# Performance work log

Hardware: AMD Instinct MI355X
Metric: run time of the kernel (lower is better)

Reference implementation:

```python
import jax, jax.numpy as jnp
import numpy as np

EPS = 1e-5
K_NN = 16

def _lin1d(x, W, b):
    # 1x1 Conv1d: x (B,C,N) -> (B,O,N)
    return jnp.einsum('oc,bcn->bon', W, x) + b[None, :, None]

def _lin2d(x, W, b):
    # 1x1 Conv2d: x (B,C,N,K) -> (B,O,N,K)
    return jnp.einsum('oc,bcnk->bonk', W, x) + b[None, :, None, None]

def _bn2d(x, gamma, beta):
    # train-mode BatchNorm2d over (B, N, K) per channel
    mean = jnp.mean(x, axis=(0, 2, 3), keepdims=True)
    var = jnp.var(x, axis=(0, 2, 3), keepdims=True)
    xh = (x - mean) * jax.lax.rsqrt(var + EPS)
    return gamma[None, :, None, None] * xh + beta[None, :, None, None]

def _knn_idx(pq, ps, k):
    # pq (B,3,N), ps (B,3,M) -> idx (B,N,K) of k nearest support points
    d2 = (jnp.sum(pq * pq, axis=1)[:, :, None]
          + jnp.sum(ps * ps, axis=1)[:, None, :]
          - 2.0 * jnp.einsum('bcn,bcm->bnm', pq, ps))
    _, idx = jax.lax.top_k(-d2, k)
    return idx

def _group(x, idx):
    # x (B,C,M), idx (B,N,K) -> (B,C,N,K)
    return jnp.take_along_axis(x[:, :, None, :], idx[:, None, :, :], axis=3)

def setup_inputs() -> dict:
    key = jax.random.key(0)
    ks = jax.random.split(key, 20)
    B, C, D, N, M, H = 4, 128, 64, 2048, 2048, 256
    s = lambda k, shape, scale: (jax.random.normal(k, shape, dtype=jnp.float32) * scale)
    return {
        'pq': s(ks[0], (B, 3, N), 1.0),
        'fq': s(ks[1], (B, C, N), 1.0),
        'ps': s(ks[2], (B, 3, M), 1.0),
        'fs': s(ks[3], (B, C, M), 1.0),
        'Wq': s(ks[4], (D, C), 0.05), 'bq': jnp.zeros((D,), jnp.float32),
        'Wk': s(ks[5], (D, C), 0.05), 'bk': jnp.zeros((D,), jnp.float32),
        'Wv': s(ks[6], (D, C), 0.05), 'bv': jnp.zeros((D,), jnp.float32),
        'Wp1': s(ks[7], (D, 3), 0.2), 'bp1': jnp.zeros((D,), jnp.float32),
        'gp': jnp.ones((D,), jnp.float32), 'btp': jnp.zeros((D,), jnp.float32),
        'Wp2': s(ks[8], (D, D), 0.05), 'bp2': jnp.zeros((D,), jnp.float32),
        'Wa1': s(ks[9], (H, D), 0.05), 'ba1': jnp.zeros((H,), jnp.float32),
        'ga': jnp.ones((H,), jnp.float32), 'bta': jnp.zeros((H,), jnp.float32),
        'Wa2': s(ks[10], (D, H), 0.05), 'ba2': jnp.zeros((D,), jnp.float32),
        'We': s(ks[11], (C, D), 0.05), 'be': jnp.zeros((C,), jnp.float32),
    }

def reference(pq, fq, ps, fs, Wq, bq, Wk, bk, Wv, bv,
              Wp1, bp1, gp, btp, Wp2, bp2,
              Wa1, ba1, ga, bta, Wa2, ba2, We, be):
    identity = fq
    q = _lin1d(fq, Wq, bq)          # (B,D,N)
    k = _lin1d(fs, Wk, bk)          # (B,D,M)
    v = _lin1d(fs, Wv, bv)          # (B,D,M)
    idx = _knn_idx(pq, ps, K_NN)    # (B,N,K)
    key_g = _group(k, idx)          # (B,D,N,K)
    qk_rel = q[:, :, :, None] - key_g
    pos_rel = pq[:, :, :, None] - _group(ps, idx)  # (B,3,N,K)
    # pos_mlp: conv-bn-relu-conv
    pe = _lin2d(pos_rel, Wp1, bp1)
    pe = jax.nn.relu(_bn2d(pe, gp, btp))
    pe = _lin2d(pe, Wp2, bp2)       # (B,D,N,K)
    # attn_mlp: conv-bn-relu-conv
    a = _lin2d(qk_rel + pe, Wa1, ba1)
    a = jax.nn.relu(_bn2d(a, ga, bta))
    a = _lin2d(a, Wa2, ba2)         # (B,D,N,K)
    attn = jax.nn.softmax(a, axis=-1)
    val = _group(v, idx) + pe       # (B,D,N,K)
    agg = jnp.einsum('bcnk,bcnk->bcn', attn, val)
    return _lin1d(agg, We, be) + identity
```

## Files before the change

kernel.cpp:

```cpp
#include <hip/hip_runtime.h>
#include <stdint.h>

#define NN 2048
#define MM 2048
#define NSAMP 131072

typedef float  fv4 __attribute__((ext_vector_type(4)));
typedef short  bfv8 __attribute__((ext_vector_type(8)));
typedef short  bfv4 __attribute__((ext_vector_type(4)));
typedef unsigned short u16;
typedef unsigned long long u64;

__device__ inline u16 f2bf(float x){
  unsigned u = __float_as_uint(x);
  return (u16)((u + 0x7FFFu + ((u>>16)&1u)) >> 16);
}
__device__ inline float bf2f(u16 u){ return __uint_as_float(((unsigned)u)<<16); }
#define MFMA16 __builtin_amdgcn_mfma_f32_16x16x32_bf16

__global__ __launch_bounds__(256) void k_prep(
    const float* __restrict__ Wq, const float* __restrict__ Wk, const float* __restrict__ Wv,
    const float* __restrict__ Wp2, const float* __restrict__ Wa2, const float* __restrict__ We,
    const float* __restrict__ ps,
    u16* __restrict__ Wqbf, u16* __restrict__ Wkbf, u16* __restrict__ Wvbf,
    u16* __restrict__ Wp2bf, u16* __restrict__ Wa2bf, u16* __restrict__ Webf,
    fv4* __restrict__ psP) {
  int gid = blockIdx.x * 256 + threadIdx.x;
  if (gid < 8192)  { Wqbf[gid] = f2bf(Wq[gid]); Wkbf[gid] = f2bf(Wk[gid]);
                     Wvbf[gid] = f2bf(Wv[gid]); Webf[gid] = f2bf(We[gid]); }
  if (gid < 4096)  Wp2bf[gid] = f2bf(Wp2[gid]);
  if (gid < 16384) Wa2bf[gid] = f2bf(Wa2[gid]);
  if (gid < 8192)  { int b = gid >> 11, m = gid & 2047;
    float x = ps[(b*3+0)*MM + m], y = ps[(b*3+1)*MM + m], z = ps[(b*3+2)*MM + m];
    fv4 p; p.x = x; p.y = y; p.z = z; p.w = x*x + y*y + z*z;
    psP[gid] = p; }
}

__global__ __launch_bounds__(256) void k_qkv(
    const float* __restrict__ fq, const float* __restrict__ fs,
    const u16* __restrict__ Wqbf, const u16* __restrict__ Wkbf, const u16* __restrict__ Wvbf,
    const float* __restrict__ bq, const float* __restrict__ bk, const float* __restrict__ bv,
    float* __restrict__ qT, float* __restrict__ kT, float* __restrict__ vT) {
  __shared__ u16 tile[2][32 * 136];
  int bid = blockIdx.x;
  int b = bid >> 6, p0 = (bid & 63) * 32;
  int t = threadIdx.x;
  int w = t >> 6, l = t & 63, lq = l >> 4, ln = l & 15;
  {
    int cq = t >> 3, n4 = (t & 7) * 4;
    #pragma unroll
    for (int it = 0; it < 4; ++it) {
      int c = it * 32 + cq;
      fv4 vq = *(const fv4*)&fq[(b*128 + c)*2048 + p0 + n4];
      fv4 vs = *(const fv4*)&fs[(b*128 + c)*2048 + p0 + n4];
      #pragma unroll
      for (int j = 0; j < 4; ++j) {
        tile[0][(n4 + j)*136 + c] = f2bf(vq[j]);
        tile[1][(n4 + j)*136 + c] = f2bf(vs[j]);
      }
    }
  }
  bfv8 A[3][4];
  #pragma unroll
  for (int mat = 0; mat < 3; ++mat) {
    const u16* W = mat == 0 ? Wqbf : (mat == 1 ? Wkbf : Wvbf);
    #pragma unroll
    for (int kk = 0; kk < 4; ++kk)
      A[mat][kk] = *(const bfv8*)(W + (w*16 + ln)*128 + kk*32 + lq*8);
  }
  __syncthreads();
  fv4 acc[3][2];
  #pragma unroll
  for (int mat = 0; mat < 3; ++mat) {
    const u16* tl = tile[mat == 0 ? 0 : 1];
    #pragma unroll
    for (int nt = 0; nt < 2; ++nt) {
      fv4 a = {0.f,0.f,0.f,0.f};
      #pragma unroll
      for (int kk = 0; kk < 4; ++kk) {
        bfv8 bb = *(const bfv8*)&tl[(nt*16 + ln)*136 + kk*32 + lq*8];
        a = MFMA16(A[mat][kk], bb, a, 0, 0, 0);
      }
      acc[mat][nt] = a;
    }
  }
  #pragma unroll
  for (int mat = 0; mat < 3; ++mat) {
    float* dst = mat == 0 ? qT : (mat == 1 ? kT : vT);
    const float* bia = mat == 0 ? bq : (mat == 1 ? bk : bv);
    fv4 bq4 = *(const fv4*)&bia[w*16 + lq*4];
    #pragma unroll
    for (int nt = 0; nt < 2; ++nt) {
      fv4 o = acc[mat][nt] + bq4;
      *(fv4*)&dst[(b*NN + p0 + nt*16 + ln)*64 + w*16 + lq*4] = o;
    }
  }
}

__global__ __launch_bounds__(128) void k_knn(
    const float* __restrict__ pq, const fv4* __restrict__ psP,
    int* __restrict__ idxb, float* __restrict__ posPart) {
  __shared__ u64 winLDS[2][64];
  __shared__ float sacc[2][9];
  int t = threadIdx.x, w = t >> 6, lane = t & 63;
  int qi = blockIdx.x * 2 + w;
  int b = qi >> 11, n = qi & 2047;
  const float* pqb = pq + b * 3 * NN;
  const fv4* psb = psP + b * 2048;
  float qx = pqb[n], qy = pqb[NN + n], qz = pqb[2 * NN + n];
  float qq = qx * qx + qy * qy + qz * qz;

  u64 A[16], Bv[16];
  #pragma unroll
  for (int j = 0; j < 16; ++j) {
    int m = lane + 64 * j;
    fv4 P = psb[m];
    float d2 = qq + P.w - 2.f * (qx * P.x + qy * P.y + qz * P.z);
    unsigned bu = __float_as_uint(d2);
    bu = (bu & 0x80000000u) ? ~bu : (bu | 0x80000000u);
    A[j] = (((u64)bu) << 32) | (unsigned)m;
  }
  #pragma unroll
  for (int j = 0; j < 16; ++j) {
    int m = lane + 64 * (j + 16);
    fv4 P = psb[m];
    float d2 = qq + P.w - 2.f * (qx * P.x + qy * P.y + qz * P.z);
    unsigned bu = __float_as_uint(d2);
    bu = (bu & 0x80000000u) ? ~bu : (bu | 0x80000000u);
    Bv[j] = (((u64)bu) << 32) | (unsigned)m;
  }
  #pragma unroll
  for (int k = 2; k <= 16; k <<= 1) {
    #pragma unroll
    for (int j = k >> 1; j > 0; j >>= 1) {
      #pragma unroll
      for (int i = 0; i < 16; ++i) {
        int l2 = i ^ j;
        if (l2 > i) {
          bool up = ((i & k) == 0);
          { u64 x = A[i], y = A[l2];
            bool sw = up ? (y < x) : (x < y);
            A[i] = sw ? y : x;  A[l2] = sw ? x : y; }
          { u64 x = Bv[i], y = Bv[l2];
            bool sw = up ? (y < x) : (x < y);
            Bv[i] = sw ? y : x; Bv[l2] = sw ? x : y; }
        }
      }
    }
  }
  #pragma unroll
  for (int i = 0; i < 16; ++i) {
    u64 y = Bv[15 - i];
    A[i] = A[i] < y ? A[i] : y;
  }
  #pragma unroll
  for (int j = 8; j > 0; j >>= 1) {
    #pragma unroll
    for (int i = 0; i < 16; ++i) {
      int l2 = i ^ j;
      if (l2 > i) {
        u64 x = A[i], y = A[l2];
        bool sw = (y < x);
        A[i] = sw ? y : x;  A[l2] = sw ? x : y;
      }
    }
  }
  for (int r = 0; r < 16; ++r) {
    u64 v = A[0];
    u64 mv = v;
    #pragma unroll
    for (int off = 1; off <= 8; off <<= 1) {
      u64 o = __shfl_xor(mv, off, 64);
      mv = o < mv ? o : mv;
    }
    bool pop = (v == mv);
    #pragma unroll
    for (int i = 0; i < 15; ++i) A[i] = pop ? A[i+1] : A[i];
    A[15] = pop ? ~0ULL : A[15];
    if ((lane & 15) == 0) winLDS[w][(lane >> 4) * 16 + r] = mv;
  }
  u64 e = winLDS[w][lane];
  #pragma unroll
  for (int k = 2; k <= 64; k <<= 1) {
    #pragma unroll
    for (int j = k >> 1; j > 0; j >>= 1) {
      u64 x = __shfl_xor(e, j, 64);
      u64 lo = e < x ? e : x, hi = e < x ? x : e;
      bool up = ((lane & k) == 0);
      bool takeLo = (((lane & j) == 0) == up);
      e = takeLo ? lo : hi;
    }
  }
  if (lane < 16) idxb[qi * 16 + lane] = (int)(e & 0xFFFFFFFFu);
  winLDS[w][lane] = e;
  float s0=0.f,s1=0.f,s2=0.f,s3=0.f,s4=0.f,s5=0.f,s6=0.f,s7=0.f,s8=0.f;
  #pragma unroll 4
  for (int r = 0; r < 16; ++r) {
    unsigned m = (unsigned)(winLDS[w][r] & 0xFFFFFFFFu);
    fv4 P = psb[m];
    float r0 = qx - P.x, r1 = qy - P.y, r2 = qz - P.z;
    s0 += r0; s1 += r1; s2 += r2;
    s3 += r0*r0; s4 += r0*r1; s5 += r0*r2;
    s6 += r1*r1; s7 += r1*r2; s8 += r2*r2;
  }
  if (lane == 0) {
    sacc[w][0]=s0; sacc[w][1]=s1; sacc[w][2]=s2; sacc[w][3]=s3; sacc[w][4]=s4;
    sacc[w][5]=s5; sacc[w][6]=s6; sacc[w][7]=s7; sacc[w][8]=s8;
  }
  __syncthreads();
  if (t < 9) posPart[blockIdx.x * 12 + t] = sacc[0][t] + sacc[1][t];
}

__global__ __launch_bounds__(256) void k_posfinal(
    const float* __restrict__ Wp1, const float* __restrict__ bp1,
    const float* __restrict__ gp, const float* __restrict__ btp,
    const float* __restrict__ posPart, float* __restrict__ Wp1f, float* __restrict__ bp1f) {
  __shared__ float red[4][9];
  __shared__ float st[9];
  int t = threadIdx.x;
  int w = t >> 6, lane = t & 63;
  float s[9];
  #pragma unroll
  for (int i = 0; i < 9; ++i) s[i] = 0.f;
  #pragma unroll
  for (int it = 0; it < 16; ++it) {
    const float* p = posPart + (it * 256 + t) * 12;
    fv4 a = *(const fv4*)p;
    fv4 b4 = *(const fv4*)(p + 4);
    float c8 = p[8];
    s[0]+=a.x; s[1]+=a.y; s[2]+=a.z; s[3]+=a.w;
    s[4]+=b4.x; s[5]+=b4.y; s[6]+=b4.z; s[7]+=b4.w;
    s[8]+=c8;
  }
  #pragma unroll
  for (int off = 32; off > 0; off >>= 1)
    #pragma unroll
    for (int i = 0; i < 9; ++i) s[i] += __shfl_xor(s[i], off, 64);
  if (lane == 0)
    #pragma unroll
    for (int i = 0; i < 9; ++i) red[w][i] = s[i];
  __syncthreads();
  if (t < 9) st[t] = red[0][t] + red[1][t] + red[2][t] + red[3][t];
  __syncthreads();
  if (t < 64) {
    int d = t;
    const float invN = 1.f / (float)NSAMP;
    float m0 = st[0]*invN, m1 = st[1]*invN, m2 = st[2]*invN;
    float C00 = st[3]*invN - m0*m0, C01 = st[4]*invN - m0*m1, C02 = st[5]*invN - m0*m2;
    float C11 = st[6]*invN - m1*m1, C12 = st[7]*invN - m1*m2, C22 = st[8]*invN - m2*m2;
    float w0 = Wp1[d*3], w1 = Wp1[d*3+1], w2 = Wp1[d*3+2];
    float mean = w0*m0 + w1*m1 + w2*m2 + bp1[d];
    float var = w0*w0*C00 + w1*w1*C11 + w2*w2*C22 + 2.f*(w0*w1*C01 + w0*w2*C02 + w1*w2*C12);
    float scale = gp[d] * rsqrtf(var + 1e-5f);
    Wp1f[d*3]   = scale * w0;
    Wp1f[d*3+1] = scale * w1;
    Wp1f[d*3+2] = scale * w2;
    bp1f[d] = btp[d] + scale * (bp1[d] - mean);
  }
}

__global__ __launch_bounds__(256) void k_ystats(
    const float* __restrict__ pq, const float* __restrict__ ps,
    const float* __restrict__ qT, const float* __restrict__ kT,
    const int* __restrict__ idxb,
    const float* __restrict__ Wp1f, const float* __restrict__ bp1f,
    const u16* __restrict__ Wp2bf, const float* __restrict__ bp2,
    float* __restrict__ Gpart, float* __restrict__ ySumPart) {
  __shared__ __align__(16) unsigned char smem[21760];
  u16*   hp   = (u16*)smem;
  u16*   y2   = (u16*)(smem + 9216);
  float* r3   = (float*)(smem + 18432);
  float* qc   = (float*)(smem + 19200);
  int*   idxA = (int*)(smem + 20224);
  float* sWp1 = (float*)(smem + 20480);
  float* sbp1 = (float*)(smem + 21248);
  float* sbp2 = (float*)(smem + 21504);

  const int t = threadIdx.x;
  const int w = t >> 6, l = t & 63, lq = l >> 4, ln = l & 15;
  const int d0 = 16*w + lq*4;

  if (t < 192) sWp1[t] = Wp1f[t];
  if (t < 64){ sbp1[t] = bp1f[t]; sbp2[t] = bp2[t]; }

  bfv8 Ape[2];
  #pragma unroll
  for (int kk = 0; kk < 2; ++kk)
    Ape[kk] = *(const bfv8*)(Wp2bf + (16*w + ln)*64 + kk*32 + lq*8);

  fv4 gacc[4];
  #pragma unroll
  for (int nt = 0; nt < 4; ++nt) gacc[nt] = (fv4){0.f,0.f,0.f,0.f};
  float ys[4] = {0.f, 0.f, 0.f, 0.f};
  __syncthreads();

  for (int ch = 0; ch < 4; ++ch) {
    const int p0 = blockIdx.x * 16 + ch * 4;
    const int b  = p0 >> 11;
    const int bN = b * 2048;
    if (t < 64) idxA[t] = idxb[p0*16 + t];
    qc[t] = qT[(p0 + (t>>6))*64 + (t & 63)];
    __syncthreads();
    if (t < 192) { int c = t >> 6, s = t & 63; int n = (p0 + (s>>4)) & 2047;
      r3[c*64 + s] = pq[(b*3+c)*NN + n] - ps[(b*3+c)*MM + idxA[s]]; }
    __syncthreads();
    { int s = t >> 2, iq = t & 3;
      float r0 = r3[s], r1 = r3[64+s], r2 = r3[128+s];
      u16 tmp[16];
      #pragma unroll
      for (int e = 0; e < 16; ++e) { int i = iq*16 + e;
        float v = sbp1[i] + sWp1[i*3]*r0 + sWp1[i*3+1]*r1 + sWp1[i*3+2]*r2;
        tmp[e] = f2bf(fmaxf(v, 0.f)); }
      *(bfv8*)&hp[s*72 + iq*16]     = *(const bfv8*)&tmp[0];
      *(bfv8*)&hp[s*72 + iq*16 + 8] = *(const bfv8*)&tmp[8];
    }
    __syncthreads();
    {
      fv4 pe[4];
      #pragma unroll
      for (int nt = 0; nt < 4; ++nt) {
        fv4 acc = {0.f,0.f,0.f,0.f};
        #pragma unroll
        for (int kk = 0; kk < 2; ++kk) {
          bfv8 bb = *(const bfv8*)&hp[(nt*16 + ln)*72 + kk*32 + lq*8];
          acc = MFMA16(Ape[kk], bb, acc, 0, 0, 0);
        }
        pe[nt] = acc;
      }
      fv4 bp2q = *(const fv4*)&sbp2[d0];
      #pragma unroll
      for (int nt = 0; nt < 4; ++nt) {
        int s = nt*16 + ln;
        int mi = idxA[s];
        fv4 kg = *(const fv4*)(kT + (bN + mi)*64 + d0);
        fv4 qv = *(const fv4*)&qc[nt*64 + d0];
        fv4 yv = qv - kg + pe[nt] + bp2q;
        #pragma unroll
        for (int r = 0; r < 4; ++r) { y2[(d0 + r)*72 + s] = f2bf(yv[r]); ys[r] += yv[r]; }
      }
    }
    __syncthreads();
    #pragma unroll
    for (int kk = 0; kk < 2; ++kk) {
      bfv8 aa = *(const bfv8*)&y2[(16*w + ln)*72 + kk*32 + lq*8];
      #pragma unroll
      for (int nt = 0; nt < 4; ++nt) {
        bfv8 bb = *(const bfv8*)&y2[(nt*16 + ln)*72 + kk*32 + lq*8];
        gacc[nt] = MFMA16(aa, bb, gacc[nt], 0, 0, 0);
      }
    }
    __syncthreads();
  }
  #pragma unroll
  for (int nt = 0; nt < 4; ++nt)
    #pragma unroll
    for (int r = 0; r < 4; ++r)
      Gpart[blockIdx.x*4096 + (16*w + lq*4 + r)*64 + nt*16 + ln] = gacc[nt][r];
  #pragma unroll
  for (int off = 1; off <= 8; off <<= 1) {
    #pragma unroll
    for (int r = 0; r < 4; ++r) ys[r] += __shfl_xor(ys[r], off, 64);
  }
  if (ln == 0) {
    #pragma unroll
    for (int r = 0; r < 4; ++r) ySumPart[blockIdx.x*64 + d0 + r] = ys[r];
  }
}

__global__ __launch_bounds__(256) void k_gred(
    const float* __restrict__ Gpart, const float* __restrict__ ySumPart,
    float* __restrict__ G, float* __restrict__ ySum) {
  __shared__ float red[256];
  int bid = blockIdx.x, t = threadIdx.x;
  int tj = t & 63, st = t >> 6;
  if (bid < 64) {
    int j = bid * 64 + tj;
    float s = 0.f;
    for (int p = st * 128; p < st * 128 + 128; ++p)
      s += Gpart[p*4096 + j];
    red[st * 64 + tj] = s;
    __syncthreads();
    if (t < 64)
      G[bid * 64 + t] = red[t] + red[64 + t] + red[128 + t] + red[192 + t];
  } else {
    float s = 0.f;
    for (int p = st * 128; p < st * 128 + 128; ++p)
      s += ySumPart[p*64 + tj];
    red[st * 64 + tj] = s;
    __syncthreads();
    if (t < 64)
      ySum[t] = red[t] + red[64 + t] + red[128 + t] + red[192 + t];
  }
}

__global__ __launch_bounds__(256) void k_attnfinal(
    const float* __restrict__ Wa1, const float* __restrict__ ba1,
    const float* __restrict__ ga, const float* __restrict__ bta,
    const float* __restrict__ ySum, const float* __restrict__ G,
    u16* __restrict__ Wa1fbf, float* __restrict__ ba1f) {
  __shared__ float red[256];
  __shared__ float mu[64];
  __shared__ float sc[1];
  int h = blockIdx.x, t = threadIdx.x;
  const float invN = 1.f / (float)NSAMP;
  if (t < 64) mu[t] = ySum[t] * invN;
  __syncthreads();
  float acc = 0.f;
  #pragma unroll
  for (int e = 0; e < 16; ++e) {
    int pi = t*16 + e, i = pi >> 6, j = pi & 63;
    float cov = G[pi]*invN - mu[i]*mu[j];
    acc += Wa1[h*64 + i] * Wa1[h*64 + j] * cov;
  }
  red[t] = acc;
  __syncthreads();
  for (int s = 128; s > 0; s >>= 1) { if (t < s) red[t] += red[t + s]; __syncthreads(); }
  float var = red[0];
  __syncthreads();
  red[t] = (t < 64) ? Wa1[h*64 + t] * mu[t] : 0.f;
  __syncthreads();
  for (int s = 128; s > 0; s >>= 1) { if (t < s) red[t] += red[t + s]; __syncthreads(); }
  if (t == 0) {
    float mean  = red[0] + ba1[h];
    float scale = ga[h] * rsqrtf(var + 1e-5f);
    sc[0] = scale;
    ba1f[h] = bta[h] + scale * (ba1[h] - mean);
  }
  __syncthreads();
  if (t < 64) Wa1fbf[h*64 + t] = f2bf(sc[0] * Wa1[h*64 + t]);
}

__global__ __launch_bounds__(256) void k_main(
    const float* __restrict__ pq, const float* __restrict__ ps,
    const float* __restrict__ qT, const float* __restrict__ kT, const float* __restrict__ vT,
    const int* __restrict__ idxb,
    const float* __restrict__ Wp1f, const float* __restrict__ bp1f,
    const u16* __restrict__ Wp2bf, const float* __restrict__ bp2,
    const u16* __restrict__ Wa1fbf, const float* __restrict__ ba1f,
    const u16* __restrict__ Wa2bf, const float* __restrict__ ba2,
    const u16* __restrict__ Webf, const float* __restrict__ be,
    const float* __restrict__ fq,
    u16* __restrict__ aggbf, float* __restrict__ out) {
  __shared__ __align__(16) unsigned char smem[65024];
  u16*   hp   = (u16*)smem;
  u16*   ha   = (u16*)smem;
  u16*   ylds = (u16*)(smem + 33792);
  float* at   = (float*)(smem + 33792);
  u16*   vt   = (u16*)(smem + 51200);
  float* r3   = (float*)(smem + 60416);
  float* qc   = (float*)(smem + 61184);
  int*   idxA = (int*)(smem + 62208);
  float* sWp1 = (float*)(smem + 62464);
  float* sbp1 = (float*)(smem + 63232);
  float* sbp2 = (float*)(smem + 63488);
  float* sba1 = (float*)(smem + 63744);
  float* sba2 = (float*)(smem + 64768);

  const int t = threadIdx.x;
  const int w = t >> 6, l = t & 63, lq = l >> 4, ln = l & 15;
  const int d0 = 16*w + lq*4;

  if (t < 192) sWp1[t] = Wp1f[t];
  if (t < 64){ sbp1[t] = bp1f[t]; sbp2[t] = bp2[t]; sba2[t] = ba2[t]; }
  sba1[t] = ba1f[t];

  bfv8 Ape[2], A1[4][2], A2[8];
  #pragma unroll
  for (int kk = 0; kk < 2; ++kk)
    Ape[kk] = *(const bfv8*)(Wp2bf + (16*w + ln)*64 + kk*32 + lq*8);
  #pragma unroll
  for (int mt = 0; mt < 4; ++mt)
    #pragma unroll
    for (int kk = 0; kk < 2; ++kk)
      A1[mt][kk] = *(const bfv8*)(Wa1fbf + (64*w + mt*16 + ln)*64 + kk*32 + lq*8);
  #pragma unroll
  for (int kk = 0; kk < 8; ++kk)
    A2[kk] = *(const bfv8*)(Wa2bf + (16*w + ln)*256 + kk*32 + lq*8);
  __syncthreads();

  for (int ch = 0; ch < 4; ++ch) {
    const int p0 = blockIdx.x * 16 + ch * 4;
    const int b  = p0 >> 11;
    const int bN = b * 2048;
    if (t < 64) idxA[t] = idxb[p0*16 + t];
    qc[t] = qT[(p0 + (t>>6))*64 + (t & 63)];
    __syncthreads();
    if (t < 192) { int c = t >> 6, s = t & 63; int n = (p0 + (s>>4)) & 2047;
      r3[c*64 + s] = pq[(b*3+c)*NN + n] - ps[(b*3+c)*MM + idxA[s]]; }
    __syncthreads();
    { int s = t >> 2, iq = t & 3;
      float r0 = r3[s], r1 = r3[64+s], r2 = r3[128+s];
      u16 tmp[16];
      #pragma unroll
      for (int e = 0; e < 16; ++e) { int i = iq*16 + e;
        float v = sbp1[i] + sWp1[i*3]*r0 + sWp1[i*3+1]*r1 + sWp1[i*3+2]*r2;
        tmp[e] = f2bf(fmaxf(v, 0.f)); }
      *(bfv8*)&hp[s*72 + iq*16]     = *(const bfv8*)&tmp[0];
      *(bfv8*)&hp[s*72 + iq*16 + 8] = *(const bfv8*)&tmp[8];
    }
    __syncthreads();
    {
      fv4 pe[4];
      #pragma unroll
      for (int nt = 0; nt < 4; ++nt) {
        fv4 acc = {0.f,0.f,0.f,0.f};
        #pragma unroll
        for (int kk = 0; kk < 2; ++kk) {
          bfv8 bb = *(const bfv8*)&hp[(nt*16 + ln)*72 + kk*32 + lq*8];
          acc = MFMA16(Ape[kk], bb, acc, 0, 0, 0);
        }
        pe[nt] = acc;
      }
      fv4 bp2q = *(const fv4*)&sbp2[d0];
      #pragma unroll
      for (int nt = 0; nt < 4; ++nt) {
        int s = nt*16 + ln;
        int mi = idxA[s];
        fv4 kg = *(const fv4*)(kT + (bN + mi)*64 + d0);
        fv4 vg = *(const fv4*)(vT + (bN + mi)*64 + d0);
        fv4 qv = *(const fv4*)&qc[nt*64 + d0];
        fv4 pv = pe[nt] + bp2q;
        fv4 yv = qv - kg + pv;
        fv4 vv = vg + pv;
        u16 yp[4], vp[4];
        #pragma unroll
        for (int r = 0; r < 4; ++r) { yp[r] = f2bf(yv[r]); vp[r] = f2bf(vv[r]); }
        *(bfv4*)&ylds[s*72 + d0] = *(const bfv4*)yp;
        *(bfv4*)&vt[s*72 + d0]   = *(const bfv4*)vp;
      }
    }
    __syncthreads();
    #pragma unroll
    for (int nt = 0; nt < 4; ++nt) {
      int s = nt*16 + ln;
      bfv8 b0 = *(const bfv8*)&ylds[s*72 + lq*8];
      bfv8 b1 = *(const bfv8*)&ylds[s*72 + 32 + lq*8];
      #pragma unroll
      for (int mt = 0; mt < 4; ++mt) {
        fv4 acc = {0.f,0.f,0.f,0.f};
        acc = MFMA16(A1[mt][0], b0, acc, 0, 0, 0);
        acc = MFMA16(A1[mt][1], b1, acc, 0, 0, 0);
        int h0 = 64*w + mt*16 + lq*4;
        fv4 bq = *(const fv4*)&sba1[h0];
        u16 hv[4];
        #pragma unroll
        for (int r = 0; r < 4; ++r) hv[r] = f2bf(fmaxf(acc[r] + bq[r], 0.f));
        *(bfv4*)&ha[s*264 + h0] = *(const bfv4*)hv;
      }
    }
    __syncthreads();
    {
      fv4 acc2[4];
      #pragma unroll
      for (int nt = 0; nt < 4; ++nt) acc2[nt] = (fv4){0.f,0.f,0.f,0.f};
      #pragma unroll
      for (int kk = 0; kk < 8; ++kk) {
        #pragma unroll
        for (int nt = 0; nt < 4; ++nt) {
          bfv8 bb = *(const bfv8*)&ha[(nt*16 + ln)*264 + kk*32 + lq*8];
          acc2[nt] = MFMA16(A2[kk], bb, acc2[nt], 0, 0, 0);
        }
      }
      fv4 ba2q = *(const fv4*)&sba2[d0];
      #pragma unroll
      for (int nt = 0; nt < 4; ++nt) {
        int s = nt*16 + ln;
        fv4 o = acc2[nt] + ba2q;
        *(fv4*)&at[s*68 + d0] = o;
      }
    }
    __syncthreads();
    {
      int dd = t & 63, pt = t >> 6;
      float a[16];
      #pragma unroll
      for (int k = 0; k < 16; ++k) a[k] = at[(pt*16 + k)*68 + dd];
      float mx = a[0];
      #pragma unroll
      for (int k = 1; k < 16; ++k) mx = fmaxf(mx, a[k]);
      float sum = 0.f, num = 0.f;
      #pragma unroll
      for (int k = 0; k < 16; ++k) {
        float e = __expf(a[k] - mx);
        sum += e;
        num += e * bf2f(vt[(pt*16 + k)*72 + dd]);
      }
      aggbf[(p0 + pt)*64 + dd] = f2bf(num / sum);
    }
    __syncthreads();
  }
  {
    const int P0 = blockIdx.x * 16;
    const int b  = P0 >> 11;
    const int n0 = P0 & 2047;
    bfv8 EA[2][2];
    #pragma unroll
    for (int mt = 0; mt < 2; ++mt)
      #pragma unroll
      for (int kk = 0; kk < 2; ++kk)
        EA[mt][kk] = *(const bfv8*)(Webf + ((w*2 + mt)*16 + ln)*64 + kk*32 + lq*8);
    const u16* bp = aggbf + (P0 + ln)*64;
    bfv8 b0 = *(const bfv8*)(bp + lq*8);
    bfv8 b1 = *(const bfv8*)(bp + 32 + lq*8);
    fv4 eacc[2];
    #pragma unroll
    for (int mt = 0; mt < 2; ++mt) {
      fv4 a = {0.f,0.f,0.f,0.f};
      a = MFMA16(EA[mt][0], b0, a, 0, 0, 0);
      a = MFMA16(EA[mt][1], b1, a, 0, 0, 0);
      eacc[mt] = a;
    }
    #pragma unroll
    for (int mt = 0; mt < 2; ++mt) {
      int c0 = (w*2 + mt)*16 + lq*4;
      fv4 bev = *(const fv4*)&be[c0];
      #pragma unroll
      for (int r = 0; r < 4; ++r) {
        int c = c0 + r;
        int o = (b*128 + c)*2048 + n0 + ln;
        out[o] = eacc[mt][r] + bev[r] + fq[o];
      }
    }
  }
}

extern "C" void kernel_launch(void* const* d_in, const int* in_sizes, int n_in,
                              void* d_out, int out_size, void* d_ws, size_t ws_size,
                              hipStream_t stream) {
  (void)in_sizes; (void)n_in; (void)out_size; (void)ws_size;
  const float* pq  = (const float*)d_in[0];
  const float* fq  = (const float*)d_in[1];
  const float* ps  = (const float*)d_in[2];
  const float* fs  = (const float*)d_in[3];
  const float* Wq  = (const float*)d_in[4];  const float* bq  = (const float*)d_in[5];
  const float* Wk  = (const float*)d_in[6];  const float* bk  = (const float*)d_in[7];
  const float* Wv  = (const float*)d_in[8];  const float* bv  = (const float*)d_in[9];
  const float* Wp1 = (const float*)d_in[10]; const float* bp1 = (const float*)d_in[11];
  const float* gp  = (const float*)d_in[12]; const float* btp = (const float*)d_in[13];
  const float* Wp2 = (const float*)d_in[14]; const float* bp2 = (const float*)d_in[15];
  const float* Wa1 = (const float*)d_in[16]; const float* ba1 = (const float*)d_in[17];
  const float* ga  = (const float*)d_in[18]; const float* bta = (const float*)d_in[19];
  const float* Wa2 = (const float*)d_in[20]; const float* ba2 = (const float*)d_in[21];
  const float* We  = (const float*)d_in[22]; const float* be  = (const float*)d_in[23];
  float* ws = (float*)d_ws;
  float* qT    = ws;
  float* kT    = ws + 524288;
  float* vT    = ws + 1048576;
  u16*   aggbf = (u16*)(ws + 1572864);
  int*   idxb  = (int*)(ws + 2097152);
  u16*   Wqbf  = (u16*)(ws + 2228224);
  u16*   Wkbf  = (u16*)(ws + 2232320);
  u16*   Wvbf  = (u16*)(ws + 2236416);
  u16*   Webf  = (u16*)(ws + 2240512);
  fv4*   psP   = (fv4*)(ws + 2244608);
  float* Wp1f  = ws + 2375680;
  float* bp1f  = ws + 2375872;
  float* ba1f  = ws + 2375936;
  float* G     = ws + 2376192;
  float* ySum  = ws + 2380288;
  float* ySumP = ws + 2380352;
  u16*   Wp2bf  = (u16*)(ws + 2413120);
  u16*   Wa2bf  = (u16*)(ws + 2415168);
  u16*   Wa1fbf = (u16*)(ws + 2423360);
  float* posPart = ws + 2431552;
  float* Gpart   = ws + 2480704;
  float* out   = (float*)d_out;

  k_prep<<<64, 256, 0, stream>>>(Wq, Wk, Wv, Wp2, Wa2, We, ps,
                                 Wqbf, Wkbf, Wvbf, Wp2bf, Wa2bf, Webf, psP);
  k_qkv<<<256, 256, 0, stream>>>(fq, fs, Wqbf, Wkbf, Wvbf, bq, bk, bv, qT, kT, vT);
  k_knn<<<4096, 128, 0, stream>>>(pq, psP, idxb, posPart);
  k_posfinal<<<1, 256, 0, stream>>>(Wp1, bp1, gp, btp, posPart, Wp1f, bp1f);
  k_ystats<<<512, 256, 0, stream>>>(pq, ps, qT, kT, idxb, Wp1f, bp1f, Wp2bf, bp2,
                                    Gpart, ySumP);
  k_gred<<<65, 256, 0, stream>>>(Gpart, ySumP, G, ySum);
  k_attnfinal<<<256, 256, 0, stream>>>(Wa1, ba1, ga, bta, ySum, G, Wa1fbf, ba1f);
  k_main<<<512, 256, 0, stream>>>(pq, ps, qT, kT, vT, idxb, Wp1f, bp1f, Wp2bf, bp2,
                                  Wa1fbf, ba1f, Wa2bf, ba2, Webf, be, fq, aggbf, out);
}
```

Before: 224.8 us.

## Replace KNN register bitonic sort with threshold filter and compact candidate sort

The KNN kernel no longer fully sorts 32 candidates per lane. Each lane now takes its single minimum, and a wave-wide bitonic sort of those minima gives the 16th smallest as a threshold. Candidates at or below the threshold are compacted into shared memory with atomics, then sorted by a 64- or 128-wide shuffle bitonic sort, with an iterative-min fallback for larger counts. Blocks now hold 4 queries, and the position statistics are reduced with shuffles. The cost is LDS atomics and data-dependent branching.

```diff
diff --git a/kernel.cpp b/kernel.cpp
--- a/kernel.cpp
+++ b/kernel.cpp
@@ -97,89 +97,35 @@
   }
 }
 
-__global__ __launch_bounds__(128) void k_knn(
+__global__ __launch_bounds__(256) void k_knn(
     const float* __restrict__ pq, const fv4* __restrict__ psP,
     int* __restrict__ idxb, float* __restrict__ posPart) {
-  __shared__ u64 winLDS[2][64];
-  __shared__ float sacc[2][9];
-  int t = threadIdx.x, w = t >> 6, lane = t & 63;
-  int qi = blockIdx.x * 2 + w;
-  int b = qi >> 11, n = qi & 2047;
+  __shared__ u64 list[4][512];
+  __shared__ u64 win[4][16];
+  __shared__ int cnt[4];
+  __shared__ float sacc[4][9];
+
+  const int t = threadIdx.x, w = t >> 6, lane = t & 63;
+  const int qi = blockIdx.x * 4 + w;
+  const int b = qi >> 11, n = qi & 2047;
   const float* pqb = pq + b * 3 * NN;
   const fv4* psb = psP + b * 2048;
-  float qx = pqb[n], qy = pqb[NN + n], qz = pqb[2 * NN + n];
-  float qq = qx * qx + qy * qy + qz * qz;
-
-  u64 A[16], Bv[16];
-  #pragma unroll
-  for (int j = 0; j < 16; ++j) {
-    int m = lane + 64 * j;
-    fv4 P = psb[m];
+  const float qx = pqb[n], qy = pqb[NN + n], qz = pqb[2 * NN + n];
+  const float qq = qx * qx + qy * qy + qz * qz;
+
+  unsigned key[32];
+  unsigned bkey = 0xFFFFFFFFu; unsigned bj = 0;
+  #pragma unroll
+  for (int j = 0; j < 32; ++j) {
+    fv4 P = psb[lane + 64*j];
     float d2 = qq + P.w - 2.f * (qx * P.x + qy * P.y + qz * P.z);
     unsigned bu = __float_as_uint(d2);
     bu = (bu & 0x80000000u) ? ~bu : (bu | 0x80000000u);
-    A[j] = (((u64)bu) << 32) | (unsigned)m;
-  }
-  #pragma unroll
-  for (int j = 0; j < 16; ++j) {
-    int m = lane + 64 * (j + 16);
-    fv4 P = psb[m];
-    float d2 = qq + P.w - 2.f * (qx * P.x + qy * P.y + qz * P.z);
-    unsigned bu = __float_as_uint(d2);
-    bu = (bu & 0x80000000u) ? ~bu : (bu | 0x80000000u);
-    Bv[j] = (((u64)bu) << 32) | (unsigned)m;
-  }
-  #pragma unroll
-  for (int k = 2; k <= 16; k <<= 1) {
-    #pragma unroll
-    for (int j = k >> 1; j > 0; j >>= 1) {
-      #pragma unroll
-      for (int i = 0; i < 16; ++i) {
-        int l2 = i ^ j;
-        if (l2 > i) {
-          bool up = ((i & k) == 0);
-          { u64 x = A[i], y = A[l2];
-            bool sw = up ? (y < x) : (x < y);
-            A[i] = sw ? y : x;  A[l2] = sw ? x : y; }
-          { u64 x = Bv[i], y = Bv[l2];
-            bool sw = up ? (y < x) : (x < y);
-            Bv[i] = sw ? y : x; Bv[l2] = sw ? x : y; }
-        }
-      }
-    }
-  }
-  #pragma unroll
-  for (int i = 0; i < 16; ++i) {
-    u64 y = Bv[15 - i];
-    A[i] = A[i] < y ? A[i] : y;
-  }
-  #pragma unroll
-  for (int j = 8; j > 0; j >>= 1) {
-    #pragma unroll
-    for (int i = 0; i < 16; ++i) {
-      int l2 = i ^ j;
-      if (l2 > i) {
-        u64 x = A[i], y = A[l2];
-        bool sw = (y < x);
-        A[i] = sw ? y : x;  A[l2] = sw ? x : y;
-      }
-    }
-  }
-  for (int r = 0; r < 16; ++r) {
-    u64 v = A[0];
-    u64 mv = v;
-    #pragma unroll
-    for (int off = 1; off <= 8; off <<= 1) {
-      u64 o = __shfl_xor(mv, off, 64);
-      mv = o < mv ? o : mv;
-    }
-    bool pop = (v == mv);
-    #pragma unroll
-    for (int i = 0; i < 15; ++i) A[i] = pop ? A[i+1] : A[i];
-    A[15] = pop ? ~0ULL : A[15];
-    if ((lane & 15) == 0) winLDS[w][(lane >> 4) * 16 + r] = mv;
-  }
-  u64 e = winLDS[w][lane];
+    key[j] = bu;
+    if (bu < bkey) { bkey = bu; bj = (unsigned)j; }
+  }
+  u64 e = (((u64)bkey) << 32) | (unsigned)(lane + 64*(int)bj);
+
   #pragma unroll
   for (int k = 2; k <= 64; k <<= 1) {
     #pragma unroll
@@ -191,24 +137,100 @@
       e = takeLo ? lo : hi;
     }
   }
-  if (lane < 16) idxb[qi * 16 + lane] = (int)(e & 0xFFFFFFFFu);
-  winLDS[w][lane] = e;
-  float s0=0.f,s1=0.f,s2=0.f,s3=0.f,s4=0.f,s5=0.f,s6=0.f,s7=0.f,s8=0.f;
-  #pragma unroll 4
-  for (int r = 0; r < 16; ++r) {
-    unsigned m = (unsigned)(winLDS[w][r] & 0xFFFFFFFFu);
+  const u64 thr = __shfl(e, 15, 64);
+  const unsigned T32 = (unsigned)(thr >> 32);
+
+  if (lane == 0) cnt[w] = 0;
+  #pragma unroll
+  for (int j = 0; j < 32; ++j) {
+    if (key[j] <= T32) {
+      int p = atomicAdd(&cnt[w], 1);
+      if (p < 512) list[w][p] = (((u64)key[j]) << 32) | (unsigned)(lane + 64*j);
+    }
+  }
+  const int C = *(volatile int*)&cnt[w];
+
+  u64 myWin = 0;
+  if (C <= 64) {
+    u64 v = (lane < C) ? list[w][lane] : ~0ULL;
+    #pragma unroll
+    for (int k = 2; k <= 64; k <<= 1) {
+      #pragma unroll
+      for (int j = k >> 1; j > 0; j >>= 1) {
+        u64 x = __shfl_xor(v, j, 64);
+        u64 lo = v < x ? v : x, hi = v < x ? x : v;
+        bool up = ((lane & k) == 0);
+        bool takeLo = (((lane & j) == 0) == up);
+        v = takeLo ? lo : hi;
+      }
+    }
+    myWin = v;
+  } else if (C <= 128) {
+    u64 e0 = list[w][lane];
+    u64 e1 = (64 + lane < C) ? list[w][64 + lane] : ~0ULL;
+    #pragma unroll
+    for (unsigned k = 2; k <= 128; k <<= 1) {
+      #pragma unroll
+      for (unsigned j = k >> 1; j > 0; j >>= 1) {
+        if (j < 64) {
+          u64 x0 = __shfl_xor(e0, (int)j, 64);
+          u64 x1 = __shfl_xor(e1, (int)j, 64);
+          bool lower = ((lane & j) == 0);
+          bool up0 = (k == 128) ? true : ((lane & k) == 0);
+          bool up1 = (k == 128) ? true : ((k == 64) ? false : ((lane & k) == 0));
+          e0 = (lower == up0) ? (e0 < x0 ? e0 : x0) : (e0 < x0 ? x0 : e0);
+          e1 = (lower == up1) ? (e1 < x1 ? e1 : x1) : (e1 < x1 ? x1 : e1);
+        } else {
+          u64 lo = e0 < e1 ? e0 : e1, hi = e0 < e1 ? e1 : e0;
+          e0 = lo; e1 = hi;
+        }
+      }
+    }
+    myWin = e0;
+  } else {
+    int Cc = C > 512 ? 512 : C;
+    for (int i = lane; i < 512; i += 64)
+      if (i >= Cc) list[w][i] = ~0ULL;
+    for (int r = 0; r < 16; ++r) {
+      u64 mv = ~0ULL;
+      #pragma unroll
+      for (int s5 = 0; s5 < 8; ++s5) {
+        u64 x = list[w][s5*64 + lane];
+        mv = x < mv ? x : mv;
+      }
+      #pragma unroll
+      for (int off = 1; off <= 32; off <<= 1) {
+        u64 x = __shfl_xor(mv, off, 64);
+        mv = x < mv ? x : mv;
+      }
+      #pragma unroll
+      for (int s5 = 0; s5 < 8; ++s5)
+        if (list[w][s5*64 + lane] == mv) list[w][s5*64 + lane] = ~0ULL;
+      if (lane == 0) win[w][r] = mv;
+    }
+    if (lane < 16) myWin = win[w][lane];
+  }
+
+  if (lane < 16) {
+    unsigned m = (unsigned)(myWin & 0xFFFFFFFFu);
+    idxb[qi * 16 + lane] = (int)m;
     fv4 P = psb[m];
     float r0 = qx - P.x, r1 = qy - P.y, r2 = qz - P.z;
-    s0 += r0; s1 += r1; s2 += r2;
-    s3 += r0*r0; s4 += r0*r1; s5 += r0*r2;
-    s6 += r1*r1; s7 += r1*r2; s8 += r2*r2;
-  }
-  if (lane == 0) {
-    sacc[w][0]=s0; sacc[w][1]=s1; sacc[w][2]=s2; sacc[w][3]=s3; sacc[w][4]=s4;
-    sacc[w][5]=s5; sacc[w][6]=s6; sacc[w][7]=s7; sacc[w][8]=s8;
-  }
-  __syncthreads();
-  if (t < 9) posPart[blockIdx.x * 12 + t] = sacc[0][t] + sacc[1][t];
+    float s[9];
+    s[0] = r0; s[1] = r1; s[2] = r2;
+    s[3] = r0*r0; s[4] = r0*r1; s[5] = r0*r2;
+    s[6] = r1*r1; s[7] = r1*r2; s[8] = r2*r2;
+    #pragma unroll
+    for (int off = 1; off <= 8; off <<= 1)
+      #pragma unroll
+      for (int i = 0; i < 9; ++i) s[i] += __shfl_xor(s[i], off, 64);
+    if (lane == 0)
+      #pragma unroll
+      for (int i = 0; i < 9; ++i) sacc[w][i] = s[i];
+  }
+  __syncthreads();
+  if (t < 9) posPart[blockIdx.x * 12 + t]
+      = sacc[0][t] + sacc[1][t] + sacc[2][t] + sacc[3][t];
 }
 
 __global__ __launch_bounds__(256) void k_posfinal(
@@ -223,7 +245,7 @@
   #pragma unroll
   for (int i = 0; i < 9; ++i) s[i] = 0.f;
   #pragma unroll
-  for (int it = 0; it < 16; ++it) {
+  for (int it = 0; it < 8; ++it) {
     const float* p = posPart + (it * 256 + t) * 12;
     fv4 a = *(const fv4*)p;
     fv4 b4 = *(const fv4*)(p + 4);
@@ -669,7 +691,7 @@
   k_prep<<<64, 256, 0, stream>>>(Wq, Wk, Wv, Wp2, Wa2, We, ps,
                                  Wqbf, Wkbf, Wvbf, Wp2bf, Wa2bf, Webf, psP);
   k_qkv<<<256, 256, 0, stream>>>(fq, fs, Wqbf, Wkbf, Wvbf, bq, bk, bv, qT, kT, vT);
-  k_knn<<<4096, 128, 0, stream>>>(pq, psP, idxb, posPart);
+  k_knn<<<2048, 256, 0, stream>>>(pq, psP, idxb, posPart);
   k_posfinal<<<1, 256, 0, stream>>>(Wp1, bp1, gp, btp, posPart, Wp1f, bp1f);
   k_ystats<<<512, 256, 0, stream>>>(pq, ps, qT, kT, idxb, Wp1f, bp1f, Wp2bf, bp2,
                                     Gpart, ySumP);
```

Result: faster. 213.3 us (-5.1%).
